# Optimization experiments

Measured on AMD Instinct MI355X. Metric: run time of the kernel, lower is better.

The kernel has to match this reference:

```python
import jax, jax.numpy as jnp
import numpy as np

B, H, W, C, NH, WS, SS = 32, 56, 56, 192, 6, 7, 3
L = H * W
N = WS * WS
HD = C // NH
EPS = 1e-3  # keras LayerNormalization default epsilon


def _rel_index(ws):
    coords = np.stack(np.meshgrid(np.arange(ws), np.arange(ws), indexing='ij')).reshape(2, -1)
    rel = (coords[:, :, None] - coords[:, None, :]).transpose(1, 2, 0)
    rel[..., 0] += ws - 1
    rel[..., 1] += ws - 1
    rel[..., 0] *= 2 * ws - 1
    return rel.sum(-1)  # (N, N) int


def _attn_mask(h, w, ws, ss):
    img = np.zeros((h, w), np.float32)
    cnt = 0
    for hs in (slice(0, -ws), slice(-ws, -ss), slice(-ss, None)):
        for wsl in (slice(0, -ws), slice(-ws, -ss), slice(-ss, None)):
            img[hs, wsl] = cnt
            cnt += 1
    mw = img.reshape(h // ws, ws, w // ws, ws).transpose(0, 2, 1, 3).reshape(-1, ws * ws)
    diff = mw[:, None, :] - mw[:, :, None]  # expand_dims(mw,1) - expand_dims(mw,2)
    return np.where(diff != 0, -100.0, 0.0).astype(np.float32)  # (nW, N, N)


REL_IDX = _rel_index(WS)
ATTN_MASK = _attn_mask(H, W, WS, SS)


def _ln(x, g, b):
    m = x.mean(-1, keepdims=True)
    v = x.var(-1, keepdims=True)
    return (x - m) / jnp.sqrt(v + EPS) * g + b


def setup_inputs() -> dict:
    key = jax.random.key(0)
    ks = jax.random.split(key, 8)
    s = 0.02
    return {
        'x': jax.random.normal(ks[0], (B, L, C), jnp.float32),
        'gamma1': jnp.ones((C,), jnp.float32),
        'beta1': jnp.zeros((C,), jnp.float32),
        'qkv_w': jax.random.normal(ks[1], (C, 3 * C), jnp.float32) * s,
        'qkv_b': jnp.zeros((3 * C,), jnp.float32),
        'proj_w': jax.random.normal(ks[2], (C, C), jnp.float32) * s,
        'proj_b': jnp.zeros((C,), jnp.float32),
        'rel_bias_table': jax.random.normal(ks[3], ((2 * WS - 1) ** 2, NH), jnp.float32) * s,
        'gamma2': jnp.ones((C,), jnp.float32),
        'beta2': jnp.zeros((C,), jnp.float32),
        'fc1_w': jax.random.normal(ks[4], (C, 4 * C), jnp.float32) * s,
        'fc1_b': jnp.zeros((4 * C,), jnp.float32),
        'fc2_w': jax.random.normal(ks[5], (4 * C, C), jnp.float32) * s,
        'fc2_b': jnp.zeros((C,), jnp.float32),
    }


def reference(x, gamma1, beta1, qkv_w, qkv_b, proj_w, proj_b, rel_bias_table,
              gamma2, beta2, fc1_w, fc1_b, fc2_w, fc2_b):
    scale = HD ** -0.5
    shortcut = x
    # norm1 + cyclic shift + window partition
    xn = _ln(x, gamma1, beta1).reshape(B, H, W, C)
    xn = jnp.roll(xn, (-SS, -SS), axis=(1, 2))
    xw = xn.reshape(B, H // WS, WS, W // WS, WS, C).transpose(0, 1, 3, 2, 4, 5).reshape(-1, N, C)
    # window attention
    qkv = (xw @ qkv_w + qkv_b).reshape(-1, N, 3, NH, HD).transpose(2, 0, 3, 1, 4)
    q, k, v = qkv[0] * scale, qkv[1], qkv[2]  # (B*nW, NH, N, HD)
    attn = jnp.einsum('whnd,whmd->whnm', q, k)
    bias = rel_bias_table[REL_IDX.reshape(-1)].reshape(N, N, NH).transpose(2, 0, 1)
    attn = attn + bias[None]
    nW = ATTN_MASK.shape[0]
    attn = attn.reshape(B, nW, NH, N, N) + jnp.asarray(ATTN_MASK)[None, :, None]
    attn = jax.nn.softmax(attn.reshape(-1, NH, N, N), axis=-1)
    out = jnp.einsum('whnm,whmd->whnd', attn, v).transpose(0, 2, 1, 3).reshape(-1, N, C)
    out = out @ proj_w + proj_b
    # window reverse + reverse shift
    xr = out.reshape(B, H // WS, W // WS, WS, WS, C).transpose(0, 1, 3, 2, 4, 5).reshape(B, H, W, C)
    xr = jnp.roll(xr, (SS, SS), axis=(1, 2)).reshape(B, L, C)
    x = shortcut + xr
    # MLP block
    y = _ln(x, gamma2, beta2)
    y = jax.nn.gelu(y @ fc1_w + fc1_b, approximate=False) @ fc2_w + fc2_b
    return x + y
```

## Files before the change

kernel.cpp:

```cpp
#include <hip/hip_runtime.h>
#include <math.h>

namespace {
constexpr int kBatch = 32, kH = 56, kW = 56, kC = 192, kNH = 6, kWS = 7, kSS = 3;
constexpr int kL   = kH * kW;
constexpr int kN   = kWS * kWS;
constexpr int kTok = kBatch * kL;
constexpr int kNWin = kTok / kN;
constexpr float kEps   = 1e-3f;
constexpr float kScale = 0.17677669529663687f;
}

typedef unsigned short u16;
typedef __attribute__((ext_vector_type(8))) short short8;
typedef __attribute__((ext_vector_type(4))) float f32x4;

__device__ __forceinline__ float bf2f(u16 u) {
    return __uint_as_float(((unsigned int)u) << 16);
}
__device__ __forceinline__ u16 f2bf(float f) {
    unsigned int x = __float_as_uint(f);
    return (u16)((x + 0x7FFFu + ((x >> 16) & 1u)) >> 16);
}
__device__ __forceinline__ float gelu_f(float x) {
    float z = 0.7978845608028654f * x * (1.0f + 0.044715f * x * x);
    float t = 1.0f - 2.0f / (1.0f + __expf(2.0f * z));
    return 0.5f * x * (1.0f + t);
}

__device__ __forceinline__ int win_row_to_tok(int idx) {
    const int win = idx / kN, n = idx - win * kN;
    const int b = win >> 6, wi = win & 63;
    const int wh = wi >> 3, ww = wi & 7;
    const int i1 = n / kWS, j1 = n - i1 * kWS;
    const int h = (wh * kWS + i1 + kSS) % kH;
    const int w = (ww * kWS + j1 + kSS) % kW;
    return b * kL + h * kW + w;
}

__global__ __launch_bounds__(256) void wprep_qkv(
    const float* __restrict__ w, u16* __restrict__ wt)
{
    const int idx = blockIdx.x * 256 + threadIdx.x;
    if (idx >= 576 * 192) return;
    const int n = idx / 192, k = idx - n * 192;
    float v = w[(size_t)k * 576 + n];
    if (n < 192) v *= kScale;
    wt[idx] = f2bf(v);
}

__global__ __launch_bounds__(256) void wprep_rest(
    const float* __restrict__ pw, const float* __restrict__ f1w,
    const float* __restrict__ f2w, u16* __restrict__ proj_t,
    u16* __restrict__ f1_t, u16* __restrict__ f2_t)
{
    int idx = blockIdx.x * 256 + threadIdx.x;
    if (idx < 36864) {
        const int n = idx / 192, k = idx - n * 192;
        proj_t[idx] = f2bf(pw[(size_t)k * 192 + n]);
        return;
    }
    idx -= 36864;
    if (idx < 147456) {
        const int n = idx / 192, k = idx - n * 192;
        f1_t[idx] = f2bf(f1w[(size_t)k * 768 + n]);
        return;
    }
    idx -= 147456;
    if (idx < 147456) {
        const int n = idx / 768, k = idx - n * 768;
        f2_t[idx] = f2bf(f2w[(size_t)k * 192 + n]);
    }
}

__global__ __launch_bounds__(256) void prep_bm(
    const float* __restrict__ btab, const float* __restrict__ qkv_b,
    float* __restrict__ T, float* __restrict__ qkv_bs)
{
    const int idx = blockIdx.x * 256 + threadIdx.x;
    if (idx < 576) qkv_bs[idx] = (idx < 192) ? qkv_b[idx] * kScale : qkv_b[idx];
    if (idx >= 4 * 6 * 49 * 49) return;
    const int m = idx % 49, n = (idx / 49) % 49;
    const int head = (idx / 2401) % 6, cls = idx / (2401 * 6);
    const int i1 = n / 7, j1 = n % 7, i2 = m / 7, j2 = m % 7;
    float v = btab[((i1 - i2 + 6) * 13 + (j1 - j2 + 6)) * kNH + head];
    const int whE = cls >> 1, wwE = cls & 1;
    const int r1 = (whE ? (i1 < 4 ? 1 : 2) : 0) * 3 + (wwE ? (j1 < 4 ? 1 : 2) : 0);
    const int r2 = (whE ? (i2 < 4 ? 1 : 2) : 0) * 3 + (wwE ? (j2 < 4 ? 1 : 2) : 0);
    if (r1 != r2) v -= 100.f;
    T[idx] = v;
}

__global__ __launch_bounds__(256) void ln_qkv(
    const float* __restrict__ x, const float* __restrict__ gamma,
    const float* __restrict__ beta,
    const u16* __restrict__ qkv_t, const float* __restrict__ qkv_bs,
    u16* __restrict__ qk_out, u16* __restrict__ vt)
{
    constexpr int Kp = 200;
    __shared__ u16 As[64 * Kp];
    __shared__ int rowsrc[64];
    const int tid  = threadIdx.x;
    const int wave = tid >> 6, lane = tid & 63;
    const int quad = lane >> 4, l15 = lane & 15;
    const int m0 = blockIdx.x * 64;

    if (tid < 64) rowsrc[tid] = win_row_to_tok(m0 + tid);
    __syncthreads();

    {
        float gv[12], bv[12];
        #pragma unroll
        for (int j = 0; j < 12; ++j) {
            gv[j] = gamma[l15 * 12 + j];
            bv[j] = beta[l15 * 12 + j];
        }
        #pragma unroll
        for (int it = 0; it < 4; ++it) {
            const int r = it * 16 + wave * 4 + quad;
            const float* xp = x + (size_t)rowsrc[r] * kC + l15 * 12;
            float4 u0 = *(const float4*)(xp);
            float4 u1 = *(const float4*)(xp + 4);
            float4 u2 = *(const float4*)(xp + 8);
            float v[12] = {u0.x, u0.y, u0.z, u0.w, u1.x, u1.y, u1.z, u1.w,
                           u2.x, u2.y, u2.z, u2.w};
            float s = 0.f, sq = 0.f;
            #pragma unroll
            for (int j = 0; j < 12; ++j) { s += v[j]; sq += v[j] * v[j]; }
            #pragma unroll
            for (int off = 1; off < 16; off <<= 1) {
                s  += __shfl_xor(s, off, 64);
                sq += __shfl_xor(sq, off, 64);
            }
            const float mean = s * (1.0f / kC);
            const float inv  = rsqrtf(sq * (1.0f / kC) - mean * mean + kEps);
            unsigned* ap = (unsigned*)&As[r * Kp + l15 * 12];
            #pragma unroll
            for (int j = 0; j < 6; ++j) {
                float a0 = (v[2 * j]     - mean) * inv * gv[2 * j]     + bv[2 * j];
                float a1 = (v[2 * j + 1] - mean) * inv * gv[2 * j + 1] + bv[2 * j + 1];
                ap[j] = (unsigned)f2bf(a0) | ((unsigned)f2bf(a1) << 16);
            }
        }
    }
    __syncthreads();

    #pragma unroll
    for (int j = 0; j < 3; ++j) {
        const int nb0 = j * 192 + wave * 48;
        const u16* Bbase = qkv_t + (size_t)(nb0 + l15) * 192 + quad * 8;
        f32x4 acc[4][3] = {};
        #pragma unroll
        for (int ks = 0; ks < 6; ++ks) {
            short8 a[4], b[3];
            #pragma unroll
            for (int i = 0; i < 4; ++i)
                a[i] = *(const short8*)&As[(i * 16 + l15) * Kp + ks * 32 + quad * 8];
            #pragma unroll
            for (int t = 0; t < 3; ++t)
                b[t] = *(const short8*)(Bbase + (size_t)t * 16 * 192 + ks * 32);
            #pragma unroll
            for (int i = 0; i < 4; ++i)
                #pragma unroll
                for (int t = 0; t < 3; ++t)
                    acc[i][t] = __builtin_amdgcn_mfma_f32_16x16x32_bf16(
                        a[i], b[t], acc[i][t], 0, 0, 0);
        }
        float bcol[3];
        #pragma unroll
        for (int t = 0; t < 3; ++t) bcol[t] = qkv_bs[nb0 + t * 16 + l15];
        #pragma unroll
        for (int i = 0; i < 4; ++i) {
            #pragma unroll
            for (int reg = 0; reg < 4; ++reg) {
                const int r = m0 + i * 16 + quad * 4 + reg;
                if (j == 2) {
                    const int win = r / kN, n = r - win * kN;
                    #pragma unroll
                    for (int t = 0; t < 3; ++t) {
                        const int d = nb0 - 384 + t * 16 + l15;
                        const size_t off =
                            ((size_t)win * 192 + d) * 64 + n;
                        vt[off] = f2bf(acc[i][t][reg] + bcol[t]);
                    }
                } else {
                    #pragma unroll
                    for (int t = 0; t < 3; ++t) {
                        const int c = nb0 + t * 16 + l15;
                        qk_out[(size_t)r * 576 + c] =
                            f2bf(acc[i][t][reg] + bcol[t]);
                    }
                }
            }
        }
    }
}

__global__ __launch_bounds__(256) void proj_mlp_fused(
    const u16* __restrict__ A,
    const u16* __restrict__ proj_t, const float* __restrict__ proj_b,
    const float* __restrict__ x,
    const float* __restrict__ gamma, const float* __restrict__ beta,
    const u16* __restrict__ f1_t, const float* __restrict__ fc1_b,
    const u16* __restrict__ f2_t, const float* __restrict__ fc2_b,
    float* __restrict__ out)
{
    constexpr int Kp = 200;
    constexpr int Hp = 200;
    __shared__ u16 As[64 * Kp];
    __shared__ u16 Hs[64 * Hp];
    __shared__ int rowdest[64];
    const int tid  = threadIdx.x;
    const int wave = tid >> 6, lane = tid & 63;
    const int quad = lane >> 4, l15 = lane & 15;
    const int m0 = blockIdx.x * 64;
    float* Hsf = (float*)Hs;

    {
        const u16* src = A + (size_t)m0 * 192;
        #pragma unroll
        for (int i = tid; i < 64 * 192 / 8; i += 256) {
            const int e = i * 8;
            const int r = e / 192, c = e - r * 192;
            *(short8*)&As[r * Kp + c] = *(const short8*)(src + e);
        }
        if (tid < 64) rowdest[tid] = win_row_to_tok(m0 + tid);
    }
    __syncthreads();

    float x1[4][3][4];
    #pragma unroll
    for (int i = 0; i < 4; ++i) {
        #pragma unroll
        for (int reg = 0; reg < 4; ++reg) {
            const float* xr = x + (size_t)rowdest[i * 16 + quad * 4 + reg] * kC
                              + wave * 48 + l15;
            #pragma unroll
            for (int t = 0; t < 3; ++t) x1[i][t][reg] = xr[t * 16];
        }
    }

    f32x4 acc[4][3] = {};
    {
        const u16* Bbase = proj_t + (size_t)(wave * 48 + l15) * 192 + quad * 8;
        #pragma unroll
        for (int ks = 0; ks < 6; ++ks) {
            short8 a[4], b[3];
            #pragma unroll
            for (int i = 0; i < 4; ++i)
                a[i] = *(const short8*)&As[(i * 16 + l15) * Kp + ks * 32 + quad * 8];
            #pragma unroll
            for (int t = 0; t < 3; ++t)
                b[t] = *(const short8*)(Bbase + (size_t)t * 16 * 192 + ks * 32);
            #pragma unroll
            for (int i = 0; i < 4; ++i)
                #pragma unroll
                for (int t = 0; t < 3; ++t)
                    acc[i][t] = __builtin_amdgcn_mfma_f32_16x16x32_bf16(
                        a[i], b[t], acc[i][t], 0, 0, 0);
        }
    }
    {
        float bcol[3];
        #pragma unroll
        for (int t = 0; t < 3; ++t) bcol[t] = proj_b[wave * 48 + t * 16 + l15];
        #pragma unroll
        for (int i = 0; i < 4; ++i)
            #pragma unroll
            for (int t = 0; t < 3; ++t)
                #pragma unroll
                for (int reg = 0; reg < 4; ++reg)
                    x1[i][t][reg] += acc[i][t][reg] + bcol[t];
    }

    #pragma unroll
    for (int i = 0; i < 4; ++i) {
        #pragma unroll
        for (int reg = 0; reg < 4; ++reg) {
            float s  = x1[i][0][reg] + x1[i][1][reg] + x1[i][2][reg];
            float sq = x1[i][0][reg] * x1[i][0][reg]
                     + x1[i][1][reg] * x1[i][1][reg]
                     + x1[i][2][reg] * x1[i][2][reg];
            #pragma unroll
            for (int off = 1; off < 16; off <<= 1) {
                s  += __shfl_xor(s, off, 64);
                sq += __shfl_xor(sq, off, 64);
            }
            if (l15 == 0) {
                const int r = i * 16 + quad * 4 + reg;
                Hsf[r * 8 + wave * 2]     = s;
                Hsf[r * 8 + wave * 2 + 1] = sq;
            }
        }
    }
    __syncthreads();
    if (tid < 64) {
        const float s  = Hsf[tid * 8] + Hsf[tid * 8 + 2] + Hsf[tid * 8 + 4] + Hsf[tid * 8 + 6];
        const float sq = Hsf[tid * 8 + 1] + Hsf[tid * 8 + 3] + Hsf[tid * 8 + 5] + Hsf[tid * 8 + 7];
        const float mean = s * (1.0f / kC);
        const float inv  = rsqrtf(sq * (1.0f / kC) - mean * mean + kEps);
        Hsf[512 + tid * 2]     = mean;
        Hsf[512 + tid * 2 + 1] = inv;
    }
    __syncthreads();
    {
        float gv[3], bv[3];
        #pragma unroll
        for (int t = 0; t < 3; ++t) {
            gv[t] = gamma[wave * 48 + t * 16 + l15];
            bv[t] = beta[wave * 48 + t * 16 + l15];
        }
        #pragma unroll
        for (int i = 0; i < 4; ++i) {
            #pragma unroll
            for (int reg = 0; reg < 4; ++reg) {
                const int r = i * 16 + quad * 4 + reg;
                const float mean = Hsf[512 + r * 2];
                const float inv  = Hsf[513 + r * 2];
                #pragma unroll
                for (int t = 0; t < 3; ++t)
                    As[r * Kp + wave * 48 + t * 16 + l15] =
                        f2bf((x1[i][t][reg] - mean) * inv * gv[t] + bv[t]);
            }
        }
    }
    __syncthreads();

    f32x4 acc2[4][3] = {};
    for (int c = 0; c < 4; ++c) {
        f32x4 acc1[4][3] = {};
        {
            const u16* B1 = f1_t + (size_t)(c * 192 + wave * 48 + l15) * 192 + quad * 8;
            #pragma unroll
            for (int ks = 0; ks < 6; ++ks) {
                short8 a[4], b[3];
                #pragma unroll
                for (int i = 0; i < 4; ++i)
                    a[i] = *(const short8*)&As[(i * 16 + l15) * Kp + ks * 32 + quad * 8];
                #pragma unroll
                for (int t = 0; t < 3; ++t)
                    b[t] = *(const short8*)(B1 + (size_t)t * 16 * 192 + ks * 32);
                #pragma unroll
                for (int i = 0; i < 4; ++i)
                    #pragma unroll
                    for (int t = 0; t < 3; ++t)
                        acc1[i][t] = __builtin_amdgcn_mfma_f32_16x16x32_bf16(
                            a[i], b[t], acc1[i][t], 0, 0, 0);
            }
        }
        __syncthreads();
        #pragma unroll
        for (int t = 0; t < 3; ++t) {
            const int cc = wave * 48 + t * 16 + l15;
            const float bb = fc1_b[c * 192 + cc];
            #pragma unroll
            for (int i = 0; i < 4; ++i) {
                #pragma unroll
                for (int reg = 0; reg < 4; ++reg) {
                    const int r = i * 16 + quad * 4 + reg;
                    Hs[r * Hp + cc] = f2bf(gelu_f(acc1[i][t][reg] + bb));
                }
            }
        }
        __syncthreads();
        {
            const u16* B2 = f2_t + (size_t)(wave * 48 + l15) * 768 + c * 192 + quad * 8;
            #pragma unroll
            for (int ks = 0; ks < 6; ++ks) {
                short8 a[4], b[3];
                #pragma unroll
                for (int i = 0; i < 4; ++i)
                    a[i] = *(const short8*)&Hs[(i * 16 + l15) * Hp + ks * 32 + quad * 8];
                #pragma unroll
                for (int t = 0; t < 3; ++t)
                    b[t] = *(const short8*)(B2 + (size_t)t * 16 * 768 + ks * 32);
                #pragma unroll
                for (int i = 0; i < 4; ++i)
                    #pragma unroll
                    for (int t = 0; t < 3; ++t)
                        acc2[i][t] = __builtin_amdgcn_mfma_f32_16x16x32_bf16(
                            a[i], b[t], acc2[i][t], 0, 0, 0);
            }
        }
    }
    #pragma unroll
    for (int t = 0; t < 3; ++t) {
        const int cc = wave * 48 + t * 16 + l15;
        const float bb = fc2_b[cc];
        #pragma unroll
        for (int i = 0; i < 4; ++i) {
            #pragma unroll
            for (int reg = 0; reg < 4; ++reg) {
                const int dr = rowdest[i * 16 + quad * 4 + reg];
                out[(size_t)dr * kC + cc] = x1[i][t][reg] + acc2[i][t][reg] + bb;
            }
        }
    }
}

__global__ __launch_bounds__(256) void attn_mfma(
    const u16* __restrict__ qkv, const u16* __restrict__ vt,
    const float* __restrict__ T, u16* __restrict__ out)
{
    __shared__ u16 Ps[4][64][72];
    const int tid = threadIdx.x;
    const int wave = tid >> 6, lane = tid & 63;
    const int quad = lane >> 4, l15 = lane & 15;
    const int pair = blockIdx.x * 4 + wave;
    const int win = pair / 6, head = pair - win * 6;
    const int wi = win & 63;
    const int cls = (((wi >> 3) == 7) ? 2 : 0) + (((wi & 7) == 7) ? 1 : 0);
    const float* Tb = T + (size_t)(cls * 6 + head) * 49 * 49;

    const u16* base = qkv + (size_t)win * 49 * 576 + head * 32 + quad * 8;
    short8 zz = {};
    short8 qa[4], kb[4];
    #pragma unroll
    for (int i = 0; i < 4; ++i) {
        const int n = i * 16 + l15;
        qa[i] = (n < 49) ? *(const short8*)(base + (size_t)n * 576) : zz;
        kb[i] = (n < 49) ? *(const short8*)(base + (size_t)n * 576 + 192) : zz;
    }
    f32x4 acc[4][4];
    #pragma unroll
    for (int i = 0; i < 4; ++i) {
        #pragma unroll
        for (int reg = 0; reg < 4; ++reg) {
            const int n = i * 16 + quad * 4 + reg;
            const bool nv = (n < 49);
            const float* Trow = Tb + (nv ? n : 0) * 49;
            #pragma unroll
            for (int j = 0; j < 3; ++j)
                acc[i][j][reg] = nv ? Trow[j * 16 + l15] : 0.f;
            acc[i][3][reg] = (nv && l15 == 0) ? Trow[48] : -30000.f;
        }
    }
    #pragma unroll
    for (int i = 0; i < 4; ++i)
        #pragma unroll
        for (int j = 0; j < 4; ++j)
            acc[i][j] = __builtin_amdgcn_mfma_f32_16x16x32_bf16(
                qa[i], kb[j], acc[i][j], 0, 0, 0);
    float rowinv[4][4];
    #pragma unroll
    for (int i = 0; i < 4; ++i) {
        #pragma unroll
        for (int reg = 0; reg < 4; ++reg) {
            const int n = i * 16 + quad * 4 + reg;
            float e0 = __expf(acc[i][0][reg]), e1 = __expf(acc[i][1][reg]);
            float e2 = __expf(acc[i][2][reg]), e3 = __expf(acc[i][3][reg]);
            float sum = e0 + e1 + e2 + e3;
            #pragma unroll
            for (int off = 1; off < 16; off <<= 1)
                sum += __shfl_xor(sum, off, 64);
            rowinv[i][reg] = 1.0f / sum;
            Ps[wave][n][0 * 16 + l15] = f2bf(e0);
            Ps[wave][n][1 * 16 + l15] = f2bf(e1);
            Ps[wave][n][2 * 16 + l15] = f2bf(e2);
            Ps[wave][n][3 * 16 + l15] = f2bf(e3);
        }
    }
    const u16* vb_base = vt + ((size_t)pair * 32 + l15) * 64 + quad * 8;
    f32x4 o[4][2] = {};
    #pragma unroll
    for (int ks = 0; ks < 2; ++ks) {
        short8 pa[4], vb[2];
        #pragma unroll
        for (int i = 0; i < 4; ++i)
            pa[i] = *(const short8*)&Ps[wave][i * 16 + l15][ks * 32 + quad * 8];
        #pragma unroll
        for (int t = 0; t < 2; ++t)
            vb[t] = *(const short8*)(vb_base + (size_t)t * 16 * 64 + ks * 32);
        #pragma unroll
        for (int i = 0; i < 4; ++i)
            #pragma unroll
            for (int t = 0; t < 2; ++t)
                o[i][t] = __builtin_amdgcn_mfma_f32_16x16x32_bf16(
                    pa[i], vb[t], o[i][t], 0, 0, 0);
    }
    u16* obase = out + (size_t)win * 49 * 192 + head * 32;
    #pragma unroll
    for (int i = 0; i < 4; ++i) {
        #pragma unroll
        for (int reg = 0; reg < 4; ++reg) {
            const int n = i * 16 + quad * 4 + reg;
            if (n < 49) {
                const float inv = rowinv[i][reg];
                obase[(size_t)n * 192 + l15]      = f2bf(o[i][0][reg] * inv);
                obase[(size_t)n * 192 + 16 + l15] = f2bf(o[i][1][reg] * inv);
            }
        }
    }
}

extern "C" void kernel_launch(void* const* d_in, const int* in_sizes, int n_in,
                              void* d_out, int out_size, void* d_ws, size_t ws_size,
                              hipStream_t stream)
{
    const float* x      = (const float*)d_in[0];
    const float* gamma1 = (const float*)d_in[1];
    const float* beta1  = (const float*)d_in[2];
    const float* qkv_w  = (const float*)d_in[3];
    const float* qkv_b  = (const float*)d_in[4];
    const float* proj_w = (const float*)d_in[5];
    const float* proj_b = (const float*)d_in[6];
    const float* btab   = (const float*)d_in[7];
    const float* gamma2 = (const float*)d_in[8];
    const float* beta2  = (const float*)d_in[9];
    const float* fc1_w  = (const float*)d_in[10];
    const float* fc1_b  = (const float*)d_in[11];
    const float* fc2_w  = (const float*)d_in[12];
    const float* fc2_b  = (const float*)d_in[13];
    float* out = (float*)d_out;

    u16* buf_a = (u16*)d_ws;
    u16* buf_b = buf_a + (size_t)kTok * 192;
    u16* qkv_t = (u16*)d_out;
    float* bm_tab = (float*)d_out + 55296;
    float* qkv_bs = bm_tab + 57624;
    u16* vT = (u16*)d_out + 230400;
    u16* wt2   = (u16*)d_ws + (size_t)kTok * 768 - 331776;
    u16* proj_t = wt2;
    u16* f1_t   = wt2 + 36864;
    u16* f2_t   = f1_t + 147456;

    wprep_qkv<<<(110592 + 255) / 256, 256, 0, stream>>>(qkv_w, qkv_t);
    prep_bm<<<(57624 + 255) / 256, 256, 0, stream>>>(btab, qkv_b, bm_tab, qkv_bs);
    ln_qkv<<<kTok / 64, 256, 0, stream>>>(
        x, gamma1, beta1, qkv_t, qkv_bs, buf_b, vT);
    attn_mfma<<<(kNWin * kNH) / 4, 256, 0, stream>>>(buf_b, vT, bm_tab, buf_a);
    wprep_rest<<<(331776 + 255) / 256, 256, 0, stream>>>(
        proj_w, fc1_w, fc2_w, proj_t, f1_t, f2_t);
    proj_mlp_fused<<<kTok / 64, 256, 0, stream>>>(
        buf_a, proj_t, proj_b, x,
        gamma2, beta2, f1_t, fc1_b, f2_t, fc2_b, out);
}
```

Before: 497.0 us.

## Fuse window attention into the projection+MLP kernel per 64-row tile

Result: slower. 646.2 us (+30.0%).

```diff
diff --git a/kernel.cpp b/kernel.cpp
--- a/kernel.cpp
+++ b/kernel.cpp
@@ -187,7 +187,7 @@
                     #pragma unroll
                     for (int t = 0; t < 3; ++t) {
                         const int c = nb0 + t * 16 + l15;
-                        qk_out[(size_t)r * 576 + c] =
+                        qk_out[(size_t)r * 384 + c] =
                             f2bf(acc[i][t][reg] + bcol[t]);
                     }
                 }
@@ -196,8 +196,10 @@
     }
 }
 
-__global__ __launch_bounds__(256) void proj_mlp_fused(
-    const u16* __restrict__ A,
+__global__ __launch_bounds__(256) void mega(
+    const u16* __restrict__ qk,
+    const u16* __restrict__ vt,
+    const float* __restrict__ T,
     const u16* __restrict__ proj_t, const float* __restrict__ proj_b,
     const float* __restrict__ x,
     const float* __restrict__ gamma, const float* __restrict__ beta,
@@ -208,23 +210,109 @@
     constexpr int Kp = 200;
     constexpr int Hp = 200;
     __shared__ u16 As[64 * Kp];
-    __shared__ u16 Hs[64 * Hp];
+    __shared__ u16 Uu[4 * 64 * 72];
     __shared__ int rowdest[64];
     const int tid  = threadIdx.x;
     const int wave = tid >> 6, lane = tid & 63;
     const int quad = lane >> 4, l15 = lane & 15;
     const int m0 = blockIdx.x * 64;
-    float* Hsf = (float*)Hs;
+    u16* Hs = Uu;
+    float* Hsf = (float*)Uu;
+
+    if (tid < 64) rowdest[tid] = win_row_to_tok(m0 + tid);
 
     {
-        const u16* src = A + (size_t)m0 * 192;
-        #pragma unroll
-        for (int i = tid; i < 64 * 192 / 8; i += 256) {
-            const int e = i * 8;
-            const int r = e / 192, c = e - r * 192;
-            *(short8*)&As[r * Kp + c] = *(const short8*)(src + e);
-        }
-        if (tid < 64) rowdest[tid] = win_row_to_tok(m0 + tid);
+        const int w0 = m0 / kN;
+        const int nunits = ((m0 + 63) / kN - w0 + 1) * 6;
+        u16* Pw = &Uu[wave * 64 * 72];
+        for (int u = wave; u < nunits; u += 4) {
+            const int win = w0 + u / 6, h = u - (u / 6) * 6;
+            const int lo  = win * kN - m0;
+            const int wi  = win & 63;
+            const int cls = (((wi >> 3) == 7) ? 2 : 0) + (((wi & 7) == 7) ? 1 : 0);
+            const float* Tb = T + (size_t)(cls * 6 + h) * 2401;
+            short8 zz = {};
+            short8 qa[4], kb[4];
+            #pragma unroll
+            for (int i = 0; i < 4; ++i) {
+                qa[i] = *(const short8*)(qk +
+                    (size_t)(m0 + i * 16 + l15) * 384 + h * 32 + quad * 8);
+                const int n = i * 16 + l15;
+                kb[i] = (n < kN) ? *(const short8*)(qk +
+                    (size_t)(win * kN + n) * 384 + 192 + h * 32 + quad * 8) : zz;
+            }
+            f32x4 acc[4][4];
+            #pragma unroll
+            for (int i = 0; i < 4; ++i) {
+                #pragma unroll
+                for (int reg = 0; reg < 4; ++reg) {
+                    const int wr = i * 16 + quad * 4 + reg - lo;
+                    const bool rv = (wr >= 0) && (wr < kN);
+                    const float* Trow = Tb + (rv ? wr : 0) * kN;
+                    #pragma unroll
+                    for (int j = 0; j < 3; ++j)
+                        acc[i][j][reg] = rv ? Trow[j * 16 + l15] : 0.f;
+                    acc[i][3][reg] = (rv && l15 == 0) ? Trow[48] : -30000.f;
+                }
+            }
+            #pragma unroll
+            for (int i = 0; i < 4; ++i)
+                #pragma unroll
+                for (int j = 0; j < 4; ++j)
+                    acc[i][j] = __builtin_amdgcn_mfma_f32_16x16x32_bf16(
+                        qa[i], kb[j], acc[i][j], 0, 0, 0);
+            float rowinv[4][4];
+            #pragma unroll
+            for (int i = 0; i < 4; ++i) {
+                #pragma unroll
+                for (int reg = 0; reg < 4; ++reg) {
+                    const int n = i * 16 + quad * 4 + reg;
+                    float e0 = __expf(acc[i][0][reg]), e1 = __expf(acc[i][1][reg]);
+                    float e2 = __expf(acc[i][2][reg]), e3 = __expf(acc[i][3][reg]);
+                    float sum = e0 + e1 + e2 + e3;
+                    #pragma unroll
+                    for (int off = 1; off < 16; off <<= 1)
+                        sum += __shfl_xor(sum, off, 64);
+                    rowinv[i][reg] = 1.0f / sum;
+                    Pw[n * 72 + 0 * 16 + l15] = f2bf(e0);
+                    Pw[n * 72 + 1 * 16 + l15] = f2bf(e1);
+                    Pw[n * 72 + 2 * 16 + l15] = f2bf(e2);
+                    Pw[n * 72 + 3 * 16 + l15] = f2bf(e3);
+                }
+            }
+            const u16* vb_base = vt + ((size_t)(win * 6 + h) * 32 + l15) * 64
+                               + quad * 8;
+            f32x4 o[4][2] = {};
+            #pragma unroll
+            for (int ks = 0; ks < 2; ++ks) {
+                short8 pa[4], vb[2];
+                #pragma unroll
+                for (int i = 0; i < 4; ++i)
+                    pa[i] = *(const short8*)&Pw[(i * 16 + l15) * 72 + ks * 32 + quad * 8];
+                #pragma unroll
+                for (int t = 0; t < 2; ++t)
+                    vb[t] = *(const short8*)(vb_base + (size_t)t * 16 * 64 + ks * 32);
+                #pragma unroll
+                for (int i = 0; i < 4; ++i)
+                    #pragma unroll
+                    for (int t = 0; t < 2; ++t)
+                        o[i][t] = __builtin_amdgcn_mfma_f32_16x16x32_bf16(
+                            pa[i], vb[t], o[i][t], 0, 0, 0);
+            }
+            #pragma unroll
+            for (int i = 0; i < 4; ++i) {
+                #pragma unroll
+                for (int reg = 0; reg < 4; ++reg) {
+                    const int lr = i * 16 + quad * 4 + reg;
+                    const int wr = lr - lo;
+                    if (wr >= 0 && wr < kN) {
+                        const float inv = rowinv[i][reg];
+                        As[lr * Kp + h * 32 + l15]      = f2bf(o[i][0][reg] * inv);
+                        As[lr * Kp + h * 32 + 16 + l15] = f2bf(o[i][1][reg] * inv);
+                    }
+                }
+            }
+        }
     }
     __syncthreads();
 
@@ -393,101 +481,6 @@
             for (int reg = 0; reg < 4; ++reg) {
                 const int dr = rowdest[i * 16 + quad * 4 + reg];
                 out[(size_t)dr * kC + cc] = x1[i][t][reg] + acc2[i][t][reg] + bb;
-            }
-        }
-    }
-}
-
-__global__ __launch_bounds__(256) void attn_mfma(
-    const u16* __restrict__ qkv, const u16* __restrict__ vt,
-    const float* __restrict__ T, u16* __restrict__ out)
-{
-    __shared__ u16 Ps[4][64][72];
-    const int tid = threadIdx.x;
-    const int wave = tid >> 6, lane = tid & 63;
-    const int quad = lane >> 4, l15 = lane & 15;
-    const int pair = blockIdx.x * 4 + wave;
-    const int win = pair / 6, head = pair - win * 6;
-    const int wi = win & 63;
-    const int cls = (((wi >> 3) == 7) ? 2 : 0) + (((wi & 7) == 7) ? 1 : 0);
-    const float* Tb = T + (size_t)(cls * 6 + head) * 49 * 49;
-
-    const u16* base = qkv + (size_t)win * 49 * 576 + head * 32 + quad * 8;
-    short8 zz = {};
-    short8 qa[4], kb[4];
-    #pragma unroll
-    for (int i = 0; i < 4; ++i) {
-        const int n = i * 16 + l15;
-        qa[i] = (n < 49) ? *(const short8*)(base + (size_t)n * 576) : zz;
-        kb[i] = (n < 49) ? *(const short8*)(base + (size_t)n * 576 + 192) : zz;
-    }
-    f32x4 acc[4][4];
-    #pragma unroll
-    for (int i = 0; i < 4; ++i) {
-        #pragma unroll
-        for (int reg = 0; reg < 4; ++reg) {
-            const int n = i * 16 + quad * 4 + reg;
-            const bool nv = (n < 49);
-            const float* Trow = Tb + (nv ? n : 0) * 49;
-            #pragma unroll
-            for (int j = 0; j < 3; ++j)
-                acc[i][j][reg] = nv ? Trow[j * 16 + l15] : 0.f;
-            acc[i][3][reg] = (nv && l15 == 0) ? Trow[48] : -30000.f;
-        }
-    }
-    #pragma unroll
-    for (int i = 0; i < 4; ++i)
-        #pragma unroll
-        for (int j = 0; j < 4; ++j)
-            acc[i][j] = __builtin_amdgcn_mfma_f32_16x16x32_bf16(
-                qa[i], kb[j], acc[i][j], 0, 0, 0);
-    float rowinv[4][4];
-    #pragma unroll
-    for (int i = 0; i < 4; ++i) {
-        #pragma unroll
-        for (int reg = 0; reg < 4; ++reg) {
-            const int n = i * 16 + quad * 4 + reg;
-            float e0 = __expf(acc[i][0][reg]), e1 = __expf(acc[i][1][reg]);
-            float e2 = __expf(acc[i][2][reg]), e3 = __expf(acc[i][3][reg]);
-            float sum = e0 + e1 + e2 + e3;
-            #pragma unroll
-            for (int off = 1; off < 16; off <<= 1)
-                sum += __shfl_xor(sum, off, 64);
-            rowinv[i][reg] = 1.0f / sum;
-            Ps[wave][n][0 * 16 + l15] = f2bf(e0);
-            Ps[wave][n][1 * 16 + l15] = f2bf(e1);
-            Ps[wave][n][2 * 16 + l15] = f2bf(e2);
-            Ps[wave][n][3 * 16 + l15] = f2bf(e3);
-        }
-    }
-    const u16* vb_base = vt + ((size_t)pair * 32 + l15) * 64 + quad * 8;
-    f32x4 o[4][2] = {};
-    #pragma unroll
-    for (int ks = 0; ks < 2; ++ks) {
-        short8 pa[4], vb[2];
-        #pragma unroll
-        for (int i = 0; i < 4; ++i)
-            pa[i] = *(const short8*)&Ps[wave][i * 16 + l15][ks * 32 + quad * 8];
-        #pragma unroll
-        for (int t = 0; t < 2; ++t)
-            vb[t] = *(const short8*)(vb_base + (size_t)t * 16 * 64 + ks * 32);
-        #pragma unroll
-        for (int i = 0; i < 4; ++i)
-            #pragma unroll
-            for (int t = 0; t < 2; ++t)
-                o[i][t] = __builtin_amdgcn_mfma_f32_16x16x32_bf16(
-                    pa[i], vb[t], o[i][t], 0, 0, 0);
-    }
-    u16* obase = out + (size_t)win * 49 * 192 + head * 32;
-    #pragma unroll
-    for (int i = 0; i < 4; ++i) {
-        #pragma unroll
-        for (int reg = 0; reg < 4; ++reg) {
-            const int n = i * 16 + quad * 4 + reg;
-            if (n < 49) {
-                const float inv = rowinv[i][reg];
-                obase[(size_t)n * 192 + l15]      = f2bf(o[i][0][reg] * inv);
-                obase[(size_t)n * 192 + 16 + l15] = f2bf(o[i][1][reg] * inv);
             }
         }
     }
@@ -513,25 +506,22 @@
     const float* fc2_b  = (const float*)d_in[13];
     float* out = (float*)d_out;
 
-    u16* buf_a = (u16*)d_ws;
-    u16* buf_b = buf_a + (size_t)kTok * 192;
-    u16* qkv_t = (u16*)d_out;
-    float* bm_tab = (float*)d_out + 55296;
+    u16* qk    = (u16*)d_ws;
+    u16* vT    = qk + (size_t)kTok * 384;
+    u16* qkv_t = vT + (size_t)2048 * 192 * 64;
+    u16* proj_t = qkv_t + 110592;
+    u16* f1_t   = proj_t + 36864;
+    u16* f2_t   = f1_t + 147456;
+    float* bm_tab = (float*)(f2_t + 147456);
     float* qkv_bs = bm_tab + 57624;
-    u16* vT = (u16*)d_out + 230400;
-    u16* wt2   = (u16*)d_ws + (size_t)kTok * 768 - 331776;
-    u16* proj_t = wt2;
-    u16* f1_t   = wt2 + 36864;
-    u16* f2_t   = f1_t + 147456;
 
     wprep_qkv<<<(110592 + 255) / 256, 256, 0, stream>>>(qkv_w, qkv_t);
     prep_bm<<<(57624 + 255) / 256, 256, 0, stream>>>(btab, qkv_b, bm_tab, qkv_bs);
-    ln_qkv<<<kTok / 64, 256, 0, stream>>>(
-        x, gamma1, beta1, qkv_t, qkv_bs, buf_b, vT);
-    attn_mfma<<<(kNWin * kNH) / 4, 256, 0, stream>>>(buf_b, vT, bm_tab, buf_a);
     wprep_rest<<<(331776 + 255) / 256, 256, 0, stream>>>(
         proj_w, fc1_w, fc2_w, proj_t, f1_t, f2_t);
-    proj_mlp_fused<<<kTok / 64, 256, 0, stream>>>(
-        buf_a, proj_t, proj_b, x,
+    ln_qkv<<<kTok / 64, 256, 0, stream>>>(
+        x, gamma1, beta1, qkv_t, qkv_bs, qk, vT);
+    mega<<<kTok / 64, 256, 0, stream>>>(
+        qk, vT, bm_tab, proj_t, proj_b, x,
         gamma2, beta2, f1_t, fc1_b, f2_t, fc2_b, out);
 }
```
